# Optimization experiments

Measured on AMD Instinct MI355X. Metric: run time of the kernel, lower is better.

## Reference

```python
import jax, jax.numpy as jnp
import numpy as np
from jax import lax

NH = 4          # num_head
DIM = 512       # attention dim
VDIM = 512      # v_dim
QDIM = 1024     # q_dim
KS = 100        # loc_kernel_size -> conv width 2*KS+1
KN = 100        # loc_kernel_num
TEMP = 0.5      # temperature
BS, TS = 8, 2048


def setup_inputs() -> dict:
    key = jax.random.key(0)
    ks = jax.random.split(key, 12)
    s = 0.05
    return {
        "dec_state": jax.random.normal(ks[0], (BS, QDIM), jnp.float32),
        "enc_feat": jax.random.normal(ks[1], (BS, TS, VDIM), jnp.float32),
        "enc_len": jax.random.randint(ks[2], (BS,), TS // 2, TS + 1).astype(jnp.int32),
        "Wq": jax.random.normal(ks[3], (NH * DIM, QDIM), jnp.float32) * s,
        "bq": jnp.zeros((NH * DIM,), jnp.float32),
        "Wk": jax.random.normal(ks[4], (NH * DIM, VDIM), jnp.float32) * s,
        "bk": jnp.zeros((NH * DIM,), jnp.float32),
        "Wv": jax.random.normal(ks[5], (NH * VDIM, VDIM), jnp.float32) * s,
        "bv": jnp.zeros((NH * VDIM,), jnp.float32),
        "loc_conv_w": jax.random.normal(ks[6], (KN, NH, 2 * KS + 1), jnp.float32) * s,
        "loc_proj_w": jax.random.normal(ks[7], (DIM, KN), jnp.float32) * s,
        "gen_w": jax.random.normal(ks[8], (1, DIM), jnp.float32) * s,
        "gen_b": jnp.zeros((1,), jnp.float32),
        "merge_w": jax.random.normal(ks[9], (VDIM, NH * VDIM), jnp.float32) * s,
        "merge_b": jnp.zeros((VDIM,), jnp.float32),
    }


def reference(dec_state, enc_feat, enc_len, Wq, bq, Wk, bk, Wv, bv,
              loc_conv_w, loc_proj_w, gen_w, gen_b, merge_w, merge_b):
    bs, ts, _ = enc_feat.shape
    # query: [bs, nh, dim]
    query = jnp.tanh(dec_state @ Wq.T + bq).reshape(bs, NH, DIM)
    # key/value: [bs, nh, ts, dim]/[bs, nh, ts, v_dim]
    key = jnp.tanh(enc_feat @ Wk.T + bk).reshape(bs, ts, NH, DIM).transpose(0, 2, 1, 3)
    value = jnp.tanh(enc_feat @ Wv.T + bv).reshape(bs, ts, NH, VDIM).transpose(0, 2, 1, 3)
    # mask & initial (uniform-over-valid) previous attention
    pos = jnp.arange(ts)
    pad_mask = pos[None, :] >= enc_len[:, None]                      # [bs, ts] True = padded
    prev = jnp.where(pad_mask, 0.0, 1.0 / enc_len[:, None].astype(jnp.float32))  # [bs, ts]
    prev_att = jnp.broadcast_to(prev[:, None, :], (bs, NH, ts))      # [bs, nh, ts]
    # location features: Conv1d(nh -> kn, width 2*KS+1, pad KS, no bias)
    conv = lax.conv_general_dilated(prev_att, loc_conv_w, (1,), [(KS, KS)],
                                    dimension_numbers=("NCH", "OIH", "NCH"))  # [bs, kn, ts]
    loc = jnp.tanh(jnp.einsum("bkt,dk->btd", conv, loc_proj_w))      # [bs, ts, dim]
    # additive energy: gen_energy(tanh(k + q + loc))
    e = jnp.tanh(key + query[:, :, None, :] + loc[:, None, :, :])    # [bs, nh, ts, dim]
    energy = jnp.einsum("bhtd,d->bht", e, gen_w[0]) + gen_b[0]
    energy = energy / TEMP
    energy = jnp.where(pad_mask[:, None, :], -jnp.inf, energy)
    attn = jax.nn.softmax(energy, axis=-1)                           # [bs, nh, ts]
    ctx = jnp.einsum("bht,bhtv->bhv", attn, value).reshape(bs, NH * VDIM)
    context = ctx @ merge_w.T + merge_b                              # [bs, v_dim]
    return attn, context
```

## Files before the change

kernel.cpp:

```cpp
#include <hip/hip_runtime.h>
#include <math.h>

#define NH 4
#define DIM 512
#define VDIM 512
#define QDIM 1024
#define KS 100
#define KN 100
#define TEMPERATURE 0.5f
#define BS 8
#define TS 2048
#define NHD (NH * DIM)

#define WS_QUERY   0
#define WS_QTAB    16384
#define WS_ENERGYP 119808
#define WS_CTX     381952
#define WS_P       398336
#define WS_F32_END 418536

typedef __bf16 bf16x8 __attribute__((ext_vector_type(8)));
typedef __bf16 bf16x4 __attribute__((ext_vector_type(4)));
typedef _Float16 f16x8 __attribute__((ext_vector_type(8)));
typedef float  f32x4  __attribute__((ext_vector_type(4)));

#define AS1(p) ((const __attribute__((address_space(1))) void*)(p))
#define AS3(p) ((__attribute__((address_space(3))) void*)(p))

__device__ __forceinline__ float fast_tanh(float x) {
    float e = __expf(2.0f * x);
    return 1.0f - __fdividef(2.0f, e + 1.0f);
}

#define NE4 (BS * TS * VDIM / 4)
#define NW4 (NHD * VDIM / 4)
#define NCVT ((NE4 + 2 * NW4) / 256)
#define NQ2  (NHD / 4)
__global__ void k_pre(const float* __restrict__ enc, const float* __restrict__ Wk,
                      const float* __restrict__ Wv, __bf16* __restrict__ enc_bf,
                      __bf16* __restrict__ wk_bf, __bf16* __restrict__ wv_bf,
                      const float* __restrict__ dec, const float* __restrict__ Wq,
                      const float* __restrict__ bq, float* __restrict__ query,
                      const float* __restrict__ convw, float* __restrict__ P) {
    const int bx = blockIdx.x;
    if (bx < NCVT) {
        int i = bx * blockDim.x + threadIdx.x;
        const float* src; __bf16* dst; int k;
        if (i < NE4)            { src = enc; dst = enc_bf; k = i; }
        else if (i < NE4 + NW4) { src = Wk;  dst = wk_bf;  k = i - NE4; }
        else                    { src = Wv;  dst = wv_bf;  k = i - NE4 - NW4; }
        float4 v = ((const float4*)src)[k];
        bf16x4 o;
        o[0] = (__bf16)v.x; o[1] = (__bf16)v.y; o[2] = (__bf16)v.z; o[3] = (__bf16)v.w;
        ((bf16x4*)dst)[k] = o;
    } else if (bx < NCVT + NQ2) {
        int o = (bx - NCVT) * 4 + (threadIdx.x >> 6);
        int lane = threadIdx.x & 63;
        const float* wr = Wq + (size_t)o * QDIM;
        float s[BS];
        #pragma unroll
        for (int b = 0; b < BS; ++b) s[b] = 0.f;
        #pragma unroll
        for (int i = 0; i < QDIM / 64; ++i) {
            float wv = wr[lane + 64 * i];
            #pragma unroll
            for (int b = 0; b < BS; ++b)
                s[b] = fmaf(wv, dec[b * QDIM + lane + 64 * i], s[b]);
        }
        #pragma unroll
        for (int off = 32; off > 0; off >>= 1)
            #pragma unroll
            for (int b = 0; b < BS; ++b) s[b] += __shfl_down(s[b], off);
        if (lane == 0) {
            float bias = bq[o];
            #pragma unroll
            for (int b = 0; b < BS; ++b) query[b * NHD + o] = tanhf(s[b] + bias);
        }
    } else {
        __shared__ float cs[KN * (2 * KS + 1)];
        int tid = threadIdx.x;
        for (int i = tid; i < KN * (2 * KS + 1); i += 256) {
            int k = i / (2 * KS + 1);
            int dt = i - k * (2 * KS + 1);
            const float* wr = convw + k * (NH * (2 * KS + 1)) + dt;
            cs[i] = wr[0] + wr[201] + wr[402] + wr[603];
        }
        __syncthreads();
        if (tid < KN) {
            float acc = 0.f;
            P[tid] = 0.f;
            const float* c = cs + tid * (2 * KS + 1);
            for (int dt = 0; dt < 2 * KS + 1; ++dt) {
                acc += c[dt];
                P[(dt + 1) * KN + tid] = acc;
            }
        }
    }
}

__global__ void k_qtab(const float* __restrict__ P, const float* __restrict__ projw,
                       float* __restrict__ Qtab, float* __restrict__ ctx) {
    int tid = threadIdx.x;
    if (blockIdx.x >= 2 * KS + 2) {
        int z = (blockIdx.x - (2 * KS + 2)) * 512 + tid;
        ((float4*)ctx)[z] = make_float4(0.f, 0.f, 0.f, 0.f);
        return;
    }
    int j = blockIdx.x;
    __shared__ float Pc[KN];
    if (tid < KN) Pc[tid] = P[j * KN + tid];
    __syncthreads();
    const float* pr = projw + tid * KN;
    float s = 0.f;
    #pragma unroll 4
    for (int k = 0; k < KN; ++k) s = fmaf(pr[k], Pc[k], s);
    Qtab[j * DIM + tid] = s;
}

__global__ __launch_bounds__(512, 4) void k_fused(
    const __bf16* __restrict__ enc_bf, const __bf16* __restrict__ wk_bf,
    const __bf16* __restrict__ wv_bf, const float* __restrict__ bk,
    const float* __restrict__ bv, const float* __restrict__ gen_w,
    const int* __restrict__ enc_len, const float* __restrict__ query,
    const float* __restrict__ Qtab, float* __restrict__ energyP,
    _Float16* __restrict__ val) {
    const int bid = blockIdx.x;
    const int b   = bid >> 8;
    const int t0  = ((bid >> 4) & 15) << 7;
    const int n0  = ((((bid >> 3) & 1) << 3) | (bid & 7)) << 7;
    const int len = enc_len[b];
    if (t0 >= len) return;
    const int tid = threadIdx.x;
    const int w = tid >> 6, lane = tid & 63;
    const int wy = w >> 2, wx = w & 3;
    const int col = lane & 15, quad = lane >> 4;
    __shared__ __bf16 smem[3 * 12288];
    f32x4 accE[4][2], accV[4][2];
    #pragma unroll
    for (int i = 0; i < 4; ++i)
        #pragma unroll
        for (int j = 0; j < 2; ++j) { accE[i][j] = (f32x4)0.f; accV[i][j] = (f32x4)0.f; }
    const int sm = tid >> 2;
    const int sj = (tid & 3) ^ (sm & 3) ^ ((sm >> 2) & 3);
    const __bf16* gpA  = enc_bf + ((size_t)b * TS + t0) * VDIM + (size_t)sm * VDIM + sj * 8;
    const __bf16* gpBk = wk_bf + ((size_t)n0 + sm) * VDIM + sj * 8;
    const __bf16* gpBv = wv_bf + ((size_t)n0 + sm) * VDIM + sj * 8;
    const int cfr = quad ^ (col & 3) ^ ((col >> 2) & 3);
    const char* pbase = (const char*)smem;
    const int offA = (((wy * 64 + col) * 4 + cfr) << 4);
    const int offB = (((wx * 32 + col) * 4 + cfr) << 4);
    #define STG(sbe)                                                               \
        __builtin_amdgcn_global_load_lds(AS1(gpA),  AS3(smem + (sbe) + w * 512), 16, 0, 0);        \
        __builtin_amdgcn_global_load_lds(AS1(gpBk), AS3(smem + (sbe) + 4096 + w * 512), 16, 0, 0); \
        __builtin_amdgcn_global_load_lds(AS1(gpBv), AS3(smem + (sbe) + 8192 + w * 512), 16, 0, 0); \
        gpA += 32; gpBk += 32; gpBv += 32;
    STG(0)
    STG(12288)
    #pragma unroll
    for (int kk = 0; kk < 16; ++kk) {
        if (kk < 15)
            asm volatile("s_waitcnt vmcnt(3) lgkmcnt(0)\n\ts_barrier" ::: "memory");
        else
            asm volatile("s_waitcnt vmcnt(0) lgkmcnt(0)\n\ts_barrier" ::: "memory");
        if (kk < 14) {
            const int sbe = ((kk + 2) % 3) * 12288;
            STG(sbe)
        }
        const int bo = (kk % 3) * 24576;
        bf16x8 af[4], bfr[2];
        #pragma unroll
        for (int i = 0; i < 4; ++i) af[i] = *(const bf16x8*)(pbase + bo + offA + i * 1024);
        #pragma unroll
        for (int j = 0; j < 2; ++j) bfr[j] = *(const bf16x8*)(pbase + bo + 8192 + offB + j * 1024);
        #pragma unroll
        for (int i = 0; i < 4; ++i)
            #pragma unroll
            for (int j = 0; j < 2; ++j)
                accE[i][j] = __builtin_amdgcn_mfma_f32_16x16x32_bf16(af[i], bfr[j], accE[i][j], 0, 0, 0);
        #pragma unroll
        for (int j = 0; j < 2; ++j) bfr[j] = *(const bf16x8*)(pbase + bo + 16384 + offB + j * 1024);
        #pragma unroll
        for (int i = 0; i < 4; ++i)
            #pragma unroll
            for (int j = 0; j < 2; ++j)
                accV[i][j] = __builtin_amdgcn_mfma_f32_16x16x32_bf16(af[i], bfr[j], accV[i][j], 0, 0, 0);
    }
    #undef STG
    __syncthreads();

    _Float16* stage = (_Float16*)smem;
    float* red = (float*)((char*)smem + 32768);

    const int h = n0 >> 9;
    const float inv_len = 1.0f / (float)len;
    float qv[2], gw[2], bkv[2], bvv[2], lI[2];
    int dj[2];
    #pragma unroll
    for (int j = 0; j < 2; ++j) {
        int n = n0 + wx * 32 + j * 16 + col;
        dj[j] = n & (DIM - 1);
        qv[j] = query[b * NHD + n];
        gw[j] = gen_w[dj[j]];
        bkv[j] = bk[n];
        bvv[j] = bv[n];
        lI[j] = fast_tanh((Qtab[(2 * KS + 1) * DIM + dj[j]] - Qtab[dj[j]]) * inv_len);
    }
    #pragma unroll
    for (int i = 0; i < 4; ++i) {
        #pragma unroll
        for (int r = 0; r < 4; ++r) {
            int tl = wy * 64 + i * 16 + quad * 4 + r;
            int t = t0 + tl;
            float l[2];
            if (t >= KS && t < len - KS) {
                #pragma unroll
                for (int j = 0; j < 2; ++j) l[j] = lI[j];
            } else {
                int lo = KS - t; if (lo < 0) lo = 0;
                int hi = KS - t + len - 1; if (hi > 2 * KS) hi = 2 * KS;
                bool has = (hi >= lo);
                #pragma unroll
                for (int j = 0; j < 2; ++j) {
                    float cv = has
                        ? (Qtab[(hi + 1) * DIM + dj[j]] - Qtab[lo * DIM + dj[j]]) * inv_len
                        : 0.f;
                    l[j] = fast_tanh(cv);
                }
            }
            float s = 0.f;
            #pragma unroll
            for (int j = 0; j < 2; ++j) {
                float key = fast_tanh(accE[i][j][r] + bkv[j]);
                float e = fast_tanh(key + qv[j] + l[j]);
                s = fmaf(e, gw[j], s);
            }
            s += __shfl_xor(s, 1); s += __shfl_xor(s, 2);
            s += __shfl_xor(s, 4); s += __shfl_xor(s, 8);
            if (col == 0) red[tl * 4 + wx] = s;
        }
    }
    #pragma unroll
    for (int j = 0; j < 2; ++j) {
        #pragma unroll
        for (int i = 0; i < 4; ++i)
            #pragma unroll
            for (int r = 0; r < 4; ++r) {
                int tl = wy * 64 + i * 16 + quad * 4 + r;
                stage[tl * 128 + wx * 32 + j * 16 + col] =
                    (_Float16)fast_tanh(accV[i][j][r] + bvv[j]);
            }
    }
    __syncthreads();
    if (tid < 128) {
        float s = red[tid * 4] + red[tid * 4 + 1] + red[tid * 4 + 2] + red[tid * 4 + 3];
        energyP[(size_t)((n0 >> 7) & 3) * 65536 + (size_t)(b * NH + h) * TS + t0 + tid] = s;
    }
    #pragma unroll
    for (int it = 0; it < 4; ++it) {
        int idx = it * 512 + tid;
        int row = idx >> 4, seg = idx & 15;
        *(float4*)((char*)(val + ((size_t)b * TS + t0 + row) * NHD + n0) + seg * 16) =
            ((const float4*)stage)[idx];
    }
}

__global__ void k_softmax(const float* __restrict__ energyP, const int* __restrict__ enc_len,
                          const float* __restrict__ gen_b, float* __restrict__ attn) {
    int bh = blockIdx.x;
    int b = bh >> 2;
    int len = enc_len[b];
    int tid = threadIdx.x;
    int w = tid >> 6, lane = tid & 63;
    const float gb = gen_b[0];
    const float* e0 = energyP + (size_t)bh * TS;
    float ev[4];
    float mx = -INFINITY;
    #pragma unroll
    for (int i = 0; i < 4; ++i) {
        int t = i * 512 + tid;
        float e = -INFINITY;
        if (t < len) {
            float s = e0[t] + e0[65536 + t] + e0[131072 + t] + e0[196608 + t];
            e = (s + gb) * (1.0f / TEMPERATURE);
        }
        ev[i] = e;
        mx = fmaxf(mx, e);
    }
    __shared__ float sred[8], ssum[8];
    #pragma unroll
    for (int off = 32; off > 0; off >>= 1) mx = fmaxf(mx, __shfl_xor(mx, off));
    if (lane == 0) sred[w] = mx;
    __syncthreads();
    #pragma unroll
    for (int k = 0; k < 8; ++k) mx = fmaxf(mx, sred[k]);
    float ls = 0.f;
    #pragma unroll
    for (int i = 0; i < 4; ++i) {
        float ex = __expf(ev[i] - mx);
        ev[i] = ex;
        ls += ex;
    }
    #pragma unroll
    for (int off = 32; off > 0; off >>= 1) ls += __shfl_xor(ls, off);
    if (lane == 0) ssum[w] = ls;
    __syncthreads();
    float tot = 0.f;
    #pragma unroll
    for (int k = 0; k < 8; ++k) tot += ssum[k];
    float inv = 1.0f / tot;
    #pragma unroll
    for (int i = 0; i < 4; ++i)
        attn[(size_t)bh * TS + i * 512 + tid] = ev[i] * inv;
}

__global__ __launch_bounds__(256) void k_ctx2(const _Float16* __restrict__ val,
                                              const float* __restrict__ attn,
                                              const int* __restrict__ enc_len,
                                              float* __restrict__ ctx) {
    const int blk = blockIdx.x;
    const int b   = blk >> 7;
    const int nc  = (blk >> 3) & 15;
    const int tsl = blk & 7;
    const int len = enc_len[b];
    const int t0  = tsl * 256;
    if (t0 >= len) return;
    const int n0 = nc * 128;
    const int h  = n0 >> 9;
    const int tid = threadIdx.x;
    const int tn = tid & 15, tr = tid >> 4;
    const float* ar = attn + (size_t)(b * NH + h) * TS;
    float acc[8];
    #pragma unroll
    for (int k = 0; k < 8; ++k) acc[k] = 0.f;
    int tend = t0 + 256; if (tend > len) tend = len;
    for (int t = t0 + tr; t < tend; t += 16) {
        float a = ar[t];
        f16x8 v = *(const f16x8*)(val + ((size_t)b * TS + t) * NHD + n0 + tn * 8);
        #pragma unroll
        for (int k = 0; k < 8; ++k) acc[k] = fmaf(a, (float)v[k], acc[k]);
    }
    __shared__ float cred[16][128];
    #pragma unroll
    for (int k = 0; k < 8; ++k) cred[tr][tn * 8 + k] = acc[k];
    __syncthreads();
    if (tid < 128) {
        float s = 0.f;
        #pragma unroll
        for (int r = 0; r < 16; ++r) s += cred[r][tid];
        atomicAdd(&ctx[(size_t)b * NHD + n0 + tid], s);
    }
}

__global__ void k_merge(const float* __restrict__ ctx, const float* __restrict__ mw,
                        const float* __restrict__ mb, float* __restrict__ out) {
    int o = blockIdx.x * 4 + (threadIdx.x >> 6);
    int lane = threadIdx.x & 63;
    const float* wr = mw + (size_t)o * NHD;
    float s[BS];
    #pragma unroll
    for (int b = 0; b < BS; ++b) s[b] = 0.f;
    #pragma unroll
    for (int i = 0; i < NHD / 64; ++i) {
        float wv = wr[lane + 64 * i];
        #pragma unroll
        for (int b = 0; b < BS; ++b)
            s[b] = fmaf(wv, ctx[b * NHD + lane + 64 * i], s[b]);
    }
    #pragma unroll
    for (int off = 32; off > 0; off >>= 1)
        #pragma unroll
        for (int b = 0; b < BS; ++b) s[b] += __shfl_down(s[b], off);
    if (lane == 0) {
        float bias = mb[o];
        #pragma unroll
        for (int b = 0; b < BS; ++b) out[b * VDIM + o] = s[b] + bias;
    }
}

extern "C" void kernel_launch(void* const* d_in, const int* in_sizes, int n_in,
                              void* d_out, int out_size, void* d_ws, size_t ws_size,
                              hipStream_t stream) {
    const float* dec     = (const float*)d_in[0];
    const float* enc     = (const float*)d_in[1];
    const int*   enc_len = (const int*)d_in[2];
    const float* Wq      = (const float*)d_in[3];
    const float* bq      = (const float*)d_in[4];
    const float* Wk      = (const float*)d_in[5];
    const float* bk      = (const float*)d_in[6];
    const float* Wv      = (const float*)d_in[7];
    const float* bv      = (const float*)d_in[8];
    const float* convw   = (const float*)d_in[9];
    const float* projw   = (const float*)d_in[10];
    const float* gen_w   = (const float*)d_in[11];
    const float* gen_b   = (const float*)d_in[12];
    const float* merge_w = (const float*)d_in[13];
    const float* merge_b = (const float*)d_in[14];

    float* out    = (float*)d_out;
    float* ws     = (float*)d_ws;
    float* query  = ws + WS_QUERY;
    float* Qtab   = ws + WS_QTAB;
    float* energyP= ws + WS_ENERGYP;
    float* ctx    = ws + WS_CTX;
    float* Pws    = ws + WS_P;
    __bf16* enc_bf = (__bf16*)((char*)d_ws + (size_t)WS_F32_END * 4);
    __bf16* wk_bf  = enc_bf + (size_t)BS * TS * VDIM;
    __bf16* wv_bf  = wk_bf + (size_t)NHD * VDIM;
    _Float16* val  = (_Float16*)(wv_bf + (size_t)NHD * VDIM);

    k_pre<<<dim3(NCVT + NQ2 + 1), dim3(256), 0, stream>>>(
        enc, Wk, Wv, enc_bf, wk_bf, wv_bf, dec, Wq, bq, query, convw, Pws);
    k_qtab<<<dim3(2 * KS + 2 + 8), dim3(512), 0, stream>>>(Pws, projw, Qtab, ctx);
    k_fused<<<dim3(2048), dim3(512), 0, stream>>>(
        enc_bf, wk_bf, wv_bf, bk, bv, gen_w, enc_len, query, Qtab, energyP, val);
    k_softmax<<<dim3(BS * NH), dim3(512), 0, stream>>>(energyP, enc_len, gen_b, out);
    k_ctx2<<<dim3(BS * 16 * 8), dim3(256), 0, stream>>>(val, out, enc_len, ctx);
    k_merge<<<dim3(VDIM / 4), dim3(256), 0, stream>>>(ctx, merge_w, merge_b, out + 65536);
}
```

Baseline: 287.7 us.

## Fuse qtab into pre kernel, merge softmax with ctx, swizzle stage LDS

Folds the location-table computation (prefix sums over conv weights times projection) into the preprocessing kernel, with each block recomputing its own prefix sum directly. Fuses softmax with the context reduction so each block recomputes the softmax for its head in-register and consumes attention from shared memory. Adds an XOR swizzle to the fp16 value staging buffer to reduce LDS bank conflicts, and raises wave priority around the MFMA section. This removes two kernel launches and the attention round-trip through global memory, at the cost of redundant softmax and prefix-sum work.

Result: slower. 298.3 us (+3.7%).

```diff
diff --git a/kernel.cpp b/kernel.cpp
--- a/kernel.cpp
+++ b/kernel.cpp
@@ -16,7 +16,6 @@
 #define WS_QTAB    16384
 #define WS_ENERGYP 119808
 #define WS_CTX     381952
-#define WS_P       398336
 #define WS_F32_END 418536
 
 typedef __bf16 bf16x8 __attribute__((ext_vector_type(8)));
@@ -36,12 +35,15 @@
 #define NW4 (NHD * VDIM / 4)
 #define NCVT ((NE4 + 2 * NW4) / 256)
 #define NQ2  (NHD / 4)
+#define NQT  (2 * KS + 2)
+#define NZB  16
 __global__ void k_pre(const float* __restrict__ enc, const float* __restrict__ Wk,
                       const float* __restrict__ Wv, __bf16* __restrict__ enc_bf,
                       __bf16* __restrict__ wk_bf, __bf16* __restrict__ wv_bf,
                       const float* __restrict__ dec, const float* __restrict__ Wq,
                       const float* __restrict__ bq, float* __restrict__ query,
-                      const float* __restrict__ convw, float* __restrict__ P) {
+                      const float* __restrict__ convw, const float* __restrict__ projw,
+                      float* __restrict__ Qtab, float* __restrict__ ctx) {
     const int bx = blockIdx.x;
     if (bx < NCVT) {
         int i = bx * blockDim.x + threadIdx.x;
@@ -76,45 +78,32 @@
             #pragma unroll
             for (int b = 0; b < BS; ++b) query[b * NHD + o] = tanhf(s[b] + bias);
         }
+    } else if (bx < NCVT + NQ2 + NQT) {
+        int j = bx - NCVT - NQ2;
+        int tid = threadIdx.x;
+        __shared__ float sk[KN];
+        if (tid < KN) {
+            const float* wr = convw + tid * (NH * (2 * KS + 1));
+            float acc = 0.f;
+            #pragma unroll 8
+            for (int dt = 0; dt < j; ++dt)
+                acc += wr[dt] + wr[201 + dt] + wr[402 + dt] + wr[603 + dt];
+            sk[tid] = acc;
+        }
+        __syncthreads();
+        #pragma unroll
+        for (int dd = 0; dd < 2; ++dd) {
+            int d = dd * 256 + tid;
+            const float* pr = projw + d * KN;
+            float s = 0.f;
+            #pragma unroll 4
+            for (int k = 0; k < KN; ++k) s = fmaf(pr[k], sk[k], s);
+            Qtab[j * DIM + d] = s;
+        }
     } else {
-        __shared__ float cs[KN * (2 * KS + 1)];
-        int tid = threadIdx.x;
-        for (int i = tid; i < KN * (2 * KS + 1); i += 256) {
-            int k = i / (2 * KS + 1);
-            int dt = i - k * (2 * KS + 1);
-            const float* wr = convw + k * (NH * (2 * KS + 1)) + dt;
-            cs[i] = wr[0] + wr[201] + wr[402] + wr[603];
-        }
-        __syncthreads();
-        if (tid < KN) {
-            float acc = 0.f;
-            P[tid] = 0.f;
-            const float* c = cs + tid * (2 * KS + 1);
-            for (int dt = 0; dt < 2 * KS + 1; ++dt) {
-                acc += c[dt];
-                P[(dt + 1) * KN + tid] = acc;
-            }
-        }
-    }
-}
-
-__global__ void k_qtab(const float* __restrict__ P, const float* __restrict__ projw,
-                       float* __restrict__ Qtab, float* __restrict__ ctx) {
-    int tid = threadIdx.x;
-    if (blockIdx.x >= 2 * KS + 2) {
-        int z = (blockIdx.x - (2 * KS + 2)) * 512 + tid;
+        int z = (bx - NCVT - NQ2 - NQT) * 256 + threadIdx.x;
         ((float4*)ctx)[z] = make_float4(0.f, 0.f, 0.f, 0.f);
-        return;
-    }
-    int j = blockIdx.x;
-    __shared__ float Pc[KN];
-    if (tid < KN) Pc[tid] = P[j * KN + tid];
-    __syncthreads();
-    const float* pr = projw + tid * KN;
-    float s = 0.f;
-    #pragma unroll 4
-    for (int k = 0; k < KN; ++k) s = fmaf(pr[k], Pc[k], s);
-    Qtab[j * DIM + tid] = s;
+    }
 }
 
 __global__ __launch_bounds__(512, 4) void k_fused(
@@ -172,6 +161,7 @@
         for (int i = 0; i < 4; ++i) af[i] = *(const bf16x8*)(pbase + bo + offA + i * 1024);
         #pragma unroll
         for (int j = 0; j < 2; ++j) bfr[j] = *(const bf16x8*)(pbase + bo + 8192 + offB + j * 1024);
+        __builtin_amdgcn_s_setprio(1);
         #pragma unroll
         for (int i = 0; i < 4; ++i)
             #pragma unroll
@@ -184,6 +174,7 @@
             #pragma unroll
             for (int j = 0; j < 2; ++j)
                 accV[i][j] = __builtin_amdgcn_mfma_f32_16x16x32_bf16(af[i], bfr[j], accV[i][j], 0, 0, 0);
+        __builtin_amdgcn_s_setprio(0);
     }
     #undef STG
     __syncthreads();
@@ -246,8 +237,9 @@
             #pragma unroll
             for (int r = 0; r < 4; ++r) {
                 int tl = wy * 64 + i * 16 + quad * 4 + r;
-                stage[tl * 128 + wx * 32 + j * 16 + col] =
-                    (_Float16)fast_tanh(accV[i][j][r] + bvv[j]);
+                int nl = wx * 32 + j * 16 + col;
+                int snl = nl ^ (((tl >> 2) & 3) << 4);
+                stage[tl * 128 + snl] = (_Float16)fast_tanh(accV[i][j][r] + bvv[j]);
             }
     }
     __syncthreads();
@@ -259,25 +251,32 @@
     for (int it = 0; it < 4; ++it) {
         int idx = it * 512 + tid;
         int row = idx >> 4, seg = idx & 15;
-        *(float4*)((char*)(val + ((size_t)b * TS + t0 + row) * NHD + n0) + seg * 16) =
-            ((const float4*)stage)[idx];
-    }
-}
-
-__global__ void k_softmax(const float* __restrict__ energyP, const int* __restrict__ enc_len,
-                          const float* __restrict__ gen_b, float* __restrict__ attn) {
-    int bh = blockIdx.x;
-    int b = bh >> 2;
-    int len = enc_len[b];
-    int tid = threadIdx.x;
-    int w = tid >> 6, lane = tid & 63;
+        int q = (row >> 2) & 3;
+        float4 vv = *(const float4*)((const char*)stage + row * 256 + ((seg * 16) ^ (q << 5)));
+        *(float4*)((char*)(val + ((size_t)b * TS + t0 + row) * NHD + n0) + seg * 16) = vv;
+    }
+}
+
+__global__ __launch_bounds__(256) void k_smctx(const float* __restrict__ energyP,
+                                               const _Float16* __restrict__ val,
+                                               const int* __restrict__ enc_len,
+                                               const float* __restrict__ gen_b,
+                                               float* __restrict__ attn,
+                                               float* __restrict__ ctx) {
+    const int blk = blockIdx.x;
+    const int b = blk >> 6, nc = (blk >> 2) & 15, tsl = blk & 3;
+    const int h = nc >> 2;
+    const int len = enc_len[b];
+    const int bh = b * NH + h;
+    const int tid = threadIdx.x;
+    const int w = tid >> 6, lane = tid & 63;
     const float gb = gen_b[0];
     const float* e0 = energyP + (size_t)bh * TS;
-    float ev[4];
+    float ev[8];
     float mx = -INFINITY;
     #pragma unroll
-    for (int i = 0; i < 4; ++i) {
-        int t = i * 512 + tid;
+    for (int i = 0; i < 8; ++i) {
+        int t = i * 256 + tid;
         float e = -INFINITY;
         if (t < len) {
             float s = e0[t] + e0[65536 + t] + e0[131072 + t] + e0[196608 + t];
@@ -286,16 +285,15 @@
         ev[i] = e;
         mx = fmaxf(mx, e);
     }
-    __shared__ float sred[8], ssum[8];
+    __shared__ float sred[4], ssum[4];
     #pragma unroll
     for (int off = 32; off > 0; off >>= 1) mx = fmaxf(mx, __shfl_xor(mx, off));
     if (lane == 0) sred[w] = mx;
     __syncthreads();
-    #pragma unroll
-    for (int k = 0; k < 8; ++k) mx = fmaxf(mx, sred[k]);
+    mx = fmaxf(fmaxf(sred[0], sred[1]), fmaxf(sred[2], sred[3]));
     float ls = 0.f;
     #pragma unroll
-    for (int i = 0; i < 4; ++i) {
+    for (int i = 0; i < 8; ++i) {
         float ex = __expf(ev[i] - mx);
         ev[i] = ex;
         ls += ex;
@@ -304,38 +302,28 @@
     for (int off = 32; off > 0; off >>= 1) ls += __shfl_xor(ls, off);
     if (lane == 0) ssum[w] = ls;
     __syncthreads();
-    float tot = 0.f;
-    #pragma unroll
-    for (int k = 0; k < 8; ++k) tot += ssum[k];
-    float inv = 1.0f / tot;
-    #pragma unroll
-    for (int i = 0; i < 4; ++i)
-        attn[(size_t)bh * TS + i * 512 + tid] = ev[i] * inv;
-}
-
-__global__ __launch_bounds__(256) void k_ctx2(const _Float16* __restrict__ val,
-                                              const float* __restrict__ attn,
-                                              const int* __restrict__ enc_len,
-                                              float* __restrict__ ctx) {
-    const int blk = blockIdx.x;
-    const int b   = blk >> 7;
-    const int nc  = (blk >> 3) & 15;
-    const int tsl = blk & 7;
-    const int len = enc_len[b];
-    const int t0  = tsl * 256;
+    float inv = 1.0f / (ssum[0] + ssum[1] + ssum[2] + ssum[3]);
+    float a0 = ev[tsl * 2] * inv;
+    float a1 = ev[tsl * 2 + 1] * inv;
+    __shared__ float sa[512];
+    sa[tid] = a0;
+    sa[256 + tid] = a1;
+    if ((nc & 3) == 0) {
+        attn[(size_t)bh * TS + tsl * 512 + tid] = a0;
+        attn[(size_t)bh * TS + tsl * 512 + 256 + tid] = a1;
+    }
+    __syncthreads();
+    const int t0 = tsl * 512;
     if (t0 >= len) return;
-    const int n0 = nc * 128;
-    const int h  = n0 >> 9;
-    const int tid = threadIdx.x;
+    int tend = t0 + 512; if (tend > len) tend = len;
     const int tn = tid & 15, tr = tid >> 4;
-    const float* ar = attn + (size_t)(b * NH + h) * TS;
     float acc[8];
     #pragma unroll
     for (int k = 0; k < 8; ++k) acc[k] = 0.f;
-    int tend = t0 + 256; if (tend > len) tend = len;
+    const _Float16* vb = val + (size_t)b * TS * NHD + (size_t)nc * 128 + tn * 8;
     for (int t = t0 + tr; t < tend; t += 16) {
-        float a = ar[t];
-        f16x8 v = *(const f16x8*)(val + ((size_t)b * TS + t) * NHD + n0 + tn * 8);
+        float a = sa[t - t0];
+        f16x8 v = *(const f16x8*)(vb + (size_t)t * NHD);
         #pragma unroll
         for (int k = 0; k < 8; ++k) acc[k] = fmaf(a, (float)v[k], acc[k]);
     }
@@ -347,7 +335,7 @@
         float s = 0.f;
         #pragma unroll
         for (int r = 0; r < 16; ++r) s += cred[r][tid];
-        atomicAdd(&ctx[(size_t)b * NHD + n0 + tid], s);
+        atomicAdd(&ctx[(size_t)b * NHD + nc * 128 + tid], s);
     }
 }
 
@@ -402,18 +390,15 @@
     float* Qtab   = ws + WS_QTAB;
     float* energyP= ws + WS_ENERGYP;
     float* ctx    = ws + WS_CTX;
-    float* Pws    = ws + WS_P;
     __bf16* enc_bf = (__bf16*)((char*)d_ws + (size_t)WS_F32_END * 4);
     __bf16* wk_bf  = enc_bf + (size_t)BS * TS * VDIM;
     __bf16* wv_bf  = wk_bf + (size_t)NHD * VDIM;
     _Float16* val  = (_Float16*)(wv_bf + (size_t)NHD * VDIM);
 
-    k_pre<<<dim3(NCVT + NQ2 + 1), dim3(256), 0, stream>>>(
-        enc, Wk, Wv, enc_bf, wk_bf, wv_bf, dec, Wq, bq, query, convw, Pws);
-    k_qtab<<<dim3(2 * KS + 2 + 8), dim3(512), 0, stream>>>(Pws, projw, Qtab, ctx);
+    k_pre<<<dim3(NCVT + NQ2 + NQT + NZB), dim3(256), 0, stream>>>(
+        enc, Wk, Wv, enc_bf, wk_bf, wv_bf, dec, Wq, bq, query, convw, projw, Qtab, ctx);
     k_fused<<<dim3(2048), dim3(512), 0, stream>>>(
         enc_bf, wk_bf, wv_bf, bk, bv, gen_w, enc_len, query, Qtab, energyP, val);
-    k_softmax<<<dim3(BS * NH), dim3(512), 0, stream>>>(energyP, enc_len, gen_b, out);
-    k_ctx2<<<dim3(BS * 16 * 8), dim3(256), 0, stream>>>(val, out, enc_len, ctx);
+    k_smctx<<<dim3(512), dim3(256), 0, stream>>>(energyP, val, enc_len, gen_b, out, ctx);
     k_merge<<<dim3(VDIM / 4), dim3(256), 0, stream>>>(ctx, merge_w, merge_b, out + 65536);
 }
```

## Fold Qtab into pre kernel, fuse softmax normalize into ctx, swizzle stage LDS

Applied to the files above, without the earlier changes.

Builds the location table and zeroes ctx inside k_pre, so the separate k_qtab launch goes away. The softmax kernel now writes only max and inverse-sum stats, and k_ctx2 recomputes the normalized attention from energyP, which avoids one write/read pass over the attention. It also XOR-swizzles the fp16 value staging buffer in LDS to cut bank conflicts, and raises wave priority around the MFMA block. The cost is that the ctx kernel now also writes the attention and recomputes exp per block, and the Qtab work runs on only 16 blocks.

New measurement: 347.2 us. 20.7% more time.

```diff
diff --git a/kernel.cpp b/kernel.cpp
--- a/kernel.cpp
+++ b/kernel.cpp
@@ -16,7 +16,7 @@
 #define WS_QTAB    16384
 #define WS_ENERGYP 119808
 #define WS_CTX     381952
-#define WS_P       398336
+#define WS_STATS   398336
 #define WS_F32_END 418536
 
 typedef __bf16 bf16x8 __attribute__((ext_vector_type(8)));
@@ -36,15 +36,76 @@
 #define NW4 (NHD * VDIM / 4)
 #define NCVT ((NE4 + 2 * NW4) / 256)
 #define NQ2  (NHD / 4)
+#define NSPEC (32 + NQ2)
 __global__ void k_pre(const float* __restrict__ enc, const float* __restrict__ Wk,
                       const float* __restrict__ Wv, __bf16* __restrict__ enc_bf,
                       __bf16* __restrict__ wk_bf, __bf16* __restrict__ wv_bf,
                       const float* __restrict__ dec, const float* __restrict__ Wq,
                       const float* __restrict__ bq, float* __restrict__ query,
-                      const float* __restrict__ convw, float* __restrict__ P) {
+                      const float* __restrict__ convw, const float* __restrict__ projw,
+                      float* __restrict__ Qtab, float* __restrict__ ctx) {
     const int bx = blockIdx.x;
-    if (bx < NCVT) {
-        int i = bx * blockDim.x + threadIdx.x;
+    const int tid = threadIdx.x;
+    if (bx < 16) {
+        __shared__ float cs[KN * (2 * KS + 1)];
+        for (int i = tid; i < KN * (2 * KS + 1); i += 256) {
+            int k = i / (2 * KS + 1);
+            int dt = i - k * (2 * KS + 1);
+            const float* wr = convw + k * (NH * (2 * KS + 1)) + dt;
+            cs[i] = wr[0] + wr[201] + wr[402] + wr[603];
+        }
+        __syncthreads();
+        if (tid < KN) {
+            float acc = 0.f;
+            float* c = cs + tid * (2 * KS + 1);
+            for (int dt = 0; dt < 2 * KS + 1; ++dt) { acc += c[dt]; c[dt] = acc; }
+        }
+        __syncthreads();
+        #pragma unroll
+        for (int jj = 0; jj < 13; ++jj) {
+            int j = bx * 13 + jj;
+            if (j >= 2 * KS + 2) break;
+            #pragma unroll
+            for (int dd = 0; dd < 2; ++dd) {
+                int d = dd * 256 + tid;
+                float s = 0.f;
+                if (j > 0) {
+                    const float* pr = projw + d * KN;
+                    #pragma unroll 4
+                    for (int k = 0; k < KN; ++k)
+                        s = fmaf(pr[k], cs[k * (2 * KS + 1) + j - 1], s);
+                }
+                Qtab[j * DIM + d] = s;
+            }
+        }
+    } else if (bx < 32) {
+        int z = (bx - 16) * 256 + tid;
+        ((float4*)ctx)[z] = make_float4(0.f, 0.f, 0.f, 0.f);
+    } else if (bx < NSPEC) {
+        int o = (bx - 32) * 4 + (tid >> 6);
+        int lane = tid & 63;
+        const float* wr = Wq + (size_t)o * QDIM;
+        float s[BS];
+        #pragma unroll
+        for (int b = 0; b < BS; ++b) s[b] = 0.f;
+        #pragma unroll
+        for (int i = 0; i < QDIM / 64; ++i) {
+            float wv = wr[lane + 64 * i];
+            #pragma unroll
+            for (int b = 0; b < BS; ++b)
+                s[b] = fmaf(wv, dec[b * QDIM + lane + 64 * i], s[b]);
+        }
+        #pragma unroll
+        for (int off = 32; off > 0; off >>= 1)
+            #pragma unroll
+            for (int b = 0; b < BS; ++b) s[b] += __shfl_down(s[b], off);
+        if (lane == 0) {
+            float bias = bq[o];
+            #pragma unroll
+            for (int b = 0; b < BS; ++b) query[b * NHD + o] = tanhf(s[b] + bias);
+        }
+    } else {
+        int i = (bx - NSPEC) * 256 + tid;
         const float* src; __bf16* dst; int k;
         if (i < NE4)            { src = enc; dst = enc_bf; k = i; }
         else if (i < NE4 + NW4) { src = Wk;  dst = wk_bf;  k = i - NE4; }
@@ -53,68 +114,7 @@
         bf16x4 o;
         o[0] = (__bf16)v.x; o[1] = (__bf16)v.y; o[2] = (__bf16)v.z; o[3] = (__bf16)v.w;
         ((bf16x4*)dst)[k] = o;
-    } else if (bx < NCVT + NQ2) {
-        int o = (bx - NCVT) * 4 + (threadIdx.x >> 6);
-        int lane = threadIdx.x & 63;
-        const float* wr = Wq + (size_t)o * QDIM;
-        float s[BS];
-        #pragma unroll
-        for (int b = 0; b < BS; ++b) s[b] = 0.f;
-        #pragma unroll
-        for (int i = 0; i < QDIM / 64; ++i) {
-            float wv = wr[lane + 64 * i];
-            #pragma unroll
-            for (int b = 0; b < BS; ++b)
-                s[b] = fmaf(wv, dec[b * QDIM + lane + 64 * i], s[b]);
-        }
-        #pragma unroll
-        for (int off = 32; off > 0; off >>= 1)
-            #pragma unroll
-            for (int b = 0; b < BS; ++b) s[b] += __shfl_down(s[b], off);
-        if (lane == 0) {
-            float bias = bq[o];
-            #pragma unroll
-            for (int b = 0; b < BS; ++b) query[b * NHD + o] = tanhf(s[b] + bias);
-        }
-    } else {
-        __shared__ float cs[KN * (2 * KS + 1)];
-        int tid = threadIdx.x;
-        for (int i = tid; i < KN * (2 * KS + 1); i += 256) {
-            int k = i / (2 * KS + 1);
-            int dt = i - k * (2 * KS + 1);
-            const float* wr = convw + k * (NH * (2 * KS + 1)) + dt;
-            cs[i] = wr[0] + wr[201] + wr[402] + wr[603];
-        }
-        __syncthreads();
-        if (tid < KN) {
-            float acc = 0.f;
-            P[tid] = 0.f;
-            const float* c = cs + tid * (2 * KS + 1);
-            for (int dt = 0; dt < 2 * KS + 1; ++dt) {
-                acc += c[dt];
-                P[(dt + 1) * KN + tid] = acc;
-            }
-        }
-    }
-}
-
-__global__ void k_qtab(const float* __restrict__ P, const float* __restrict__ projw,
-                       float* __restrict__ Qtab, float* __restrict__ ctx) {
-    int tid = threadIdx.x;
-    if (blockIdx.x >= 2 * KS + 2) {
-        int z = (blockIdx.x - (2 * KS + 2)) * 512 + tid;
-        ((float4*)ctx)[z] = make_float4(0.f, 0.f, 0.f, 0.f);
-        return;
-    }
-    int j = blockIdx.x;
-    __shared__ float Pc[KN];
-    if (tid < KN) Pc[tid] = P[j * KN + tid];
-    __syncthreads();
-    const float* pr = projw + tid * KN;
-    float s = 0.f;
-    #pragma unroll 4
-    for (int k = 0; k < KN; ++k) s = fmaf(pr[k], Pc[k], s);
-    Qtab[j * DIM + tid] = s;
+    }
 }
 
 __global__ __launch_bounds__(512, 4) void k_fused(
@@ -172,6 +172,7 @@
         for (int i = 0; i < 4; ++i) af[i] = *(const bf16x8*)(pbase + bo + offA + i * 1024);
         #pragma unroll
         for (int j = 0; j < 2; ++j) bfr[j] = *(const bf16x8*)(pbase + bo + 8192 + offB + j * 1024);
+        __builtin_amdgcn_s_setprio(1);
         #pragma unroll
         for (int i = 0; i < 4; ++i)
             #pragma unroll
@@ -184,6 +185,7 @@
             #pragma unroll
             for (int j = 0; j < 2; ++j)
                 accV[i][j] = __builtin_amdgcn_mfma_f32_16x16x32_bf16(af[i], bfr[j], accV[i][j], 0, 0, 0);
+        __builtin_amdgcn_s_setprio(0);
     }
     #undef STG
     __syncthreads();
@@ -246,8 +248,9 @@
             #pragma unroll
             for (int r = 0; r < 4; ++r) {
                 int tl = wy * 64 + i * 16 + quad * 4 + r;
-                stage[tl * 128 + wx * 32 + j * 16 + col] =
-                    (_Float16)fast_tanh(accV[i][j][r] + bvv[j]);
+                int nl = wx * 32 + j * 16 + col;
+                int snl = nl ^ (((tl >> 2) & 3) << 4);
+                stage[tl * 128 + snl] = (_Float16)fast_tanh(accV[i][j][r] + bvv[j]);
             }
     }
     __syncthreads();
@@ -259,13 +262,14 @@
     for (int it = 0; it < 4; ++it) {
         int idx = it * 512 + tid;
         int row = idx >> 4, seg = idx & 15;
-        *(float4*)((char*)(val + ((size_t)b * TS + t0 + row) * NHD + n0) + seg * 16) =
-            ((const float4*)stage)[idx];
-    }
-}
-
-__global__ void k_softmax(const float* __restrict__ energyP, const int* __restrict__ enc_len,
-                          const float* __restrict__ gen_b, float* __restrict__ attn) {
+        int q = (row >> 2) & 3;
+        float4 vv = *(const float4*)((const char*)stage + row * 256 + ((seg * 16) ^ (q << 5)));
+        *(float4*)((char*)(val + ((size_t)b * TS + t0 + row) * NHD + n0) + seg * 16) = vv;
+    }
+}
+
+__global__ void k_stats(const float* __restrict__ energyP, const int* __restrict__ enc_len,
+                        const float* __restrict__ gen_b, float2* __restrict__ stats) {
     int bh = blockIdx.x;
     int b = bh >> 2;
     int len = enc_len[b];
@@ -295,27 +299,25 @@
     for (int k = 0; k < 8; ++k) mx = fmaxf(mx, sred[k]);
     float ls = 0.f;
     #pragma unroll
-    for (int i = 0; i < 4; ++i) {
-        float ex = __expf(ev[i] - mx);
-        ev[i] = ex;
-        ls += ex;
-    }
+    for (int i = 0; i < 4; ++i) ls += __expf(ev[i] - mx);
     #pragma unroll
     for (int off = 32; off > 0; off >>= 1) ls += __shfl_xor(ls, off);
     if (lane == 0) ssum[w] = ls;
     __syncthreads();
-    float tot = 0.f;
-    #pragma unroll
-    for (int k = 0; k < 8; ++k) tot += ssum[k];
-    float inv = 1.0f / tot;
-    #pragma unroll
-    for (int i = 0; i < 4; ++i)
-        attn[(size_t)bh * TS + i * 512 + tid] = ev[i] * inv;
+    if (tid == 0) {
+        float tot = 0.f;
+        #pragma unroll
+        for (int k = 0; k < 8; ++k) tot += ssum[k];
+        stats[bh] = make_float2(mx, 1.0f / tot);
+    }
 }
 
 __global__ __launch_bounds__(256) void k_ctx2(const _Float16* __restrict__ val,
-                                              const float* __restrict__ attn,
+                                              const float* __restrict__ energyP,
+                                              const float2* __restrict__ stats,
                                               const int* __restrict__ enc_len,
+                                              const float* __restrict__ gen_b,
+                                              float* __restrict__ attn,
                                               float* __restrict__ ctx) {
     const int blk = blockIdx.x;
     const int b   = blk >> 7;
@@ -323,21 +325,35 @@
     const int tsl = blk & 7;
     const int len = enc_len[b];
     const int t0  = tsl * 256;
+    const int h   = nc >> 2;
+    const int bh  = b * NH + h;
+    const int tid = threadIdx.x;
+    const float2 st = stats[bh];
+    const float gb = gen_b[0];
+    const float* e0 = energyP + (size_t)bh * TS;
+    int t = t0 + tid;
+    float a = 0.f;
+    if (t < len) {
+        float s = e0[t] + e0[65536 + t] + e0[131072 + t] + e0[196608 + t];
+        a = __expf((s + gb) * (1.0f / TEMPERATURE) - st.x) * st.y;
+    }
+    if ((nc & 3) == 0) attn[(size_t)bh * TS + t] = a;
     if (t0 >= len) return;
+    __shared__ float sa[256];
+    sa[tid] = a;
+    __syncthreads();
     const int n0 = nc * 128;
-    const int h  = n0 >> 9;
-    const int tid = threadIdx.x;
     const int tn = tid & 15, tr = tid >> 4;
-    const float* ar = attn + (size_t)(b * NH + h) * TS;
     float acc[8];
     #pragma unroll
     for (int k = 0; k < 8; ++k) acc[k] = 0.f;
     int tend = t0 + 256; if (tend > len) tend = len;
-    for (int t = t0 + tr; t < tend; t += 16) {
-        float a = ar[t];
-        f16x8 v = *(const f16x8*)(val + ((size_t)b * TS + t) * NHD + n0 + tn * 8);
-        #pragma unroll
-        for (int k = 0; k < 8; ++k) acc[k] = fmaf(a, (float)v[k], acc[k]);
+    const _Float16* vb = val + (size_t)b * TS * NHD + n0 + tn * 8;
+    for (int tt = t0 + tr; tt < tend; tt += 16) {
+        float av = sa[tt - t0];
+        f16x8 v = *(const f16x8*)(vb + (size_t)tt * NHD);
+        #pragma unroll
+        for (int k = 0; k < 8; ++k) acc[k] = fmaf(av, (float)v[k], acc[k]);
     }
     __shared__ float cred[16][128];
     #pragma unroll
@@ -402,18 +418,18 @@
     float* Qtab   = ws + WS_QTAB;
     float* energyP= ws + WS_ENERGYP;
     float* ctx    = ws + WS_CTX;
-    float* Pws    = ws + WS_P;
+    float2* stats = (float2*)(ws + WS_STATS);
     __bf16* enc_bf = (__bf16*)((char*)d_ws + (size_t)WS_F32_END * 4);
     __bf16* wk_bf  = enc_bf + (size_t)BS * TS * VDIM;
     __bf16* wv_bf  = wk_bf + (size_t)NHD * VDIM;
     _Float16* val  = (_Float16*)(wv_bf + (size_t)NHD * VDIM);
 
-    k_pre<<<dim3(NCVT + NQ2 + 1), dim3(256), 0, stream>>>(
-        enc, Wk, Wv, enc_bf, wk_bf, wv_bf, dec, Wq, bq, query, convw, Pws);
-    k_qtab<<<dim3(2 * KS + 2 + 8), dim3(512), 0, stream>>>(Pws, projw, Qtab, ctx);
+    k_pre<<<dim3(NSPEC + NCVT), dim3(256), 0, stream>>>(
+        enc, Wk, Wv, enc_bf, wk_bf, wv_bf, dec, Wq, bq, query, convw, projw, Qtab, ctx);
     k_fused<<<dim3(2048), dim3(512), 0, stream>>>(
         enc_bf, wk_bf, wv_bf, bk, bv, gen_w, enc_len, query, Qtab, energyP, val);
-    k_softmax<<<dim3(BS * NH), dim3(512), 0, stream>>>(energyP, enc_len, gen_b, out);
-    k_ctx2<<<dim3(BS * 16 * 8), dim3(256), 0, stream>>>(val, out, enc_len, ctx);
+    k_stats<<<dim3(BS * NH), dim3(512), 0, stream>>>(energyP, enc_len, gen_b, stats);
+    k_ctx2<<<dim3(BS * 16 * 8), dim3(256), 0, stream>>>(
+        val, energyP, stats, enc_len, gen_b, out, ctx);
     k_merge<<<dim3(VDIM / 4), dim3(256), 0, stream>>>(ctx, merge_w, merge_b, out + 65536);
 }
```

## Reorder prep blocks, skip padded conversion, add MFMA priority and LDS swizzle

Applied to the files above, without the earlier changes.

The prep kernel is reordered so the long serial conv-prefix block and the query projection blocks launch first, and the conv prefix is computed directly from global memory without a shared staging pass. The bf16 conversion of encoder features now skips padded timesteps past enc_len, cutting memory traffic. The fused kernel raises wave priority around the MFMA section and XOR-swizzles the fp16 value staging buffer in LDS to reduce bank conflicts. Skipping conversion leaves stale bf16 data for padded rows, which is acceptable only if downstream results for those rows are masked.

Result: slower. 306.9 us (+6.6%).

```diff
diff --git a/kernel.cpp b/kernel.cpp
--- a/kernel.cpp
+++ b/kernel.cpp
@@ -41,60 +41,59 @@
                       __bf16* __restrict__ wk_bf, __bf16* __restrict__ wv_bf,
                       const float* __restrict__ dec, const float* __restrict__ Wq,
                       const float* __restrict__ bq, float* __restrict__ query,
-                      const float* __restrict__ convw, float* __restrict__ P) {
+                      const float* __restrict__ convw, float* __restrict__ P,
+                      const int* __restrict__ enc_len) {
     const int bx = blockIdx.x;
-    if (bx < NCVT) {
-        int i = bx * blockDim.x + threadIdx.x;
+    const int tid = threadIdx.x;
+    if (bx == 0) {
+        if (tid < KN) {
+            const float* wr = convw + tid * (NH * (2 * KS + 1));
+            float acc = 0.f;
+            P[tid] = 0.f;
+            #pragma unroll 4
+            for (int dt = 0; dt < 2 * KS + 1; ++dt) {
+                acc += wr[dt] + wr[201 + dt] + wr[402 + dt] + wr[603 + dt];
+                P[(dt + 1) * KN + tid] = acc;
+            }
+        }
+    } else if (bx <= NQ2) {
+        int o = (bx - 1) * 4 + (tid >> 6);
+        int lane = tid & 63;
+        const float* wr = Wq + (size_t)o * QDIM;
+        float s[BS];
+        #pragma unroll
+        for (int b = 0; b < BS; ++b) s[b] = 0.f;
+        #pragma unroll
+        for (int i = 0; i < QDIM / 64; ++i) {
+            float wv = wr[lane + 64 * i];
+            #pragma unroll
+            for (int b = 0; b < BS; ++b)
+                s[b] = fmaf(wv, dec[b * QDIM + lane + 64 * i], s[b]);
+        }
+        #pragma unroll
+        for (int off = 32; off > 0; off >>= 1)
+            #pragma unroll
+            for (int b = 0; b < BS; ++b) s[b] += __shfl_down(s[b], off);
+        if (lane == 0) {
+            float bias = bq[o];
+            #pragma unroll
+            for (int b = 0; b < BS; ++b) query[b * NHD + o] = tanhf(s[b] + bias);
+        }
+    } else {
+        int i = (bx - 1 - NQ2) * 256 + tid;
         const float* src; __bf16* dst; int k;
-        if (i < NE4)            { src = enc; dst = enc_bf; k = i; }
+        if (i < NE4) {
+            int b = i >> 18;
+            int t = (i >> 7) & (TS - 1);
+            if (t >= enc_len[b]) return;
+            src = enc; dst = enc_bf; k = i;
+        }
         else if (i < NE4 + NW4) { src = Wk;  dst = wk_bf;  k = i - NE4; }
         else                    { src = Wv;  dst = wv_bf;  k = i - NE4 - NW4; }
         float4 v = ((const float4*)src)[k];
         bf16x4 o;
         o[0] = (__bf16)v.x; o[1] = (__bf16)v.y; o[2] = (__bf16)v.z; o[3] = (__bf16)v.w;
         ((bf16x4*)dst)[k] = o;
-    } else if (bx < NCVT + NQ2) {
-        int o = (bx - NCVT) * 4 + (threadIdx.x >> 6);
-        int lane = threadIdx.x & 63;
-        const float* wr = Wq + (size_t)o * QDIM;
-        float s[BS];
-        #pragma unroll
-        for (int b = 0; b < BS; ++b) s[b] = 0.f;
-        #pragma unroll
-        for (int i = 0; i < QDIM / 64; ++i) {
-            float wv = wr[lane + 64 * i];
-            #pragma unroll
-            for (int b = 0; b < BS; ++b)
-                s[b] = fmaf(wv, dec[b * QDIM + lane + 64 * i], s[b]);
-        }
-        #pragma unroll
-        for (int off = 32; off > 0; off >>= 1)
-            #pragma unroll
-            for (int b = 0; b < BS; ++b) s[b] += __shfl_down(s[b], off);
-        if (lane == 0) {
-            float bias = bq[o];
-            #pragma unroll
-            for (int b = 0; b < BS; ++b) query[b * NHD + o] = tanhf(s[b] + bias);
-        }
-    } else {
-        __shared__ float cs[KN * (2 * KS + 1)];
-        int tid = threadIdx.x;
-        for (int i = tid; i < KN * (2 * KS + 1); i += 256) {
-            int k = i / (2 * KS + 1);
-            int dt = i - k * (2 * KS + 1);
-            const float* wr = convw + k * (NH * (2 * KS + 1)) + dt;
-            cs[i] = wr[0] + wr[201] + wr[402] + wr[603];
-        }
-        __syncthreads();
-        if (tid < KN) {
-            float acc = 0.f;
-            P[tid] = 0.f;
-            const float* c = cs + tid * (2 * KS + 1);
-            for (int dt = 0; dt < 2 * KS + 1; ++dt) {
-                acc += c[dt];
-                P[(dt + 1) * KN + tid] = acc;
-            }
-        }
     }
 }
 
@@ -172,6 +171,7 @@
         for (int i = 0; i < 4; ++i) af[i] = *(const bf16x8*)(pbase + bo + offA + i * 1024);
         #pragma unroll
         for (int j = 0; j < 2; ++j) bfr[j] = *(const bf16x8*)(pbase + bo + 8192 + offB + j * 1024);
+        __builtin_amdgcn_s_setprio(1);
         #pragma unroll
         for (int i = 0; i < 4; ++i)
             #pragma unroll
@@ -184,6 +184,7 @@
             #pragma unroll
             for (int j = 0; j < 2; ++j)
                 accV[i][j] = __builtin_amdgcn_mfma_f32_16x16x32_bf16(af[i], bfr[j], accV[i][j], 0, 0, 0);
+        __builtin_amdgcn_s_setprio(0);
     }
     #undef STG
     __syncthreads();
@@ -246,8 +247,9 @@
             #pragma unroll
             for (int r = 0; r < 4; ++r) {
                 int tl = wy * 64 + i * 16 + quad * 4 + r;
-                stage[tl * 128 + wx * 32 + j * 16 + col] =
-                    (_Float16)fast_tanh(accV[i][j][r] + bvv[j]);
+                int nl = wx * 32 + j * 16 + col;
+                int snl = nl ^ (((tl >> 2) & 3) << 4);
+                stage[tl * 128 + snl] = (_Float16)fast_tanh(accV[i][j][r] + bvv[j]);
             }
     }
     __syncthreads();
@@ -259,8 +261,9 @@
     for (int it = 0; it < 4; ++it) {
         int idx = it * 512 + tid;
         int row = idx >> 4, seg = idx & 15;
-        *(float4*)((char*)(val + ((size_t)b * TS + t0 + row) * NHD + n0) + seg * 16) =
-            ((const float4*)stage)[idx];
+        int q = (row >> 2) & 3;
+        float4 vv = *(const float4*)((const char*)stage + row * 256 + ((seg * 16) ^ (q << 5)));
+        *(float4*)((char*)(val + ((size_t)b * TS + t0 + row) * NHD + n0) + seg * 16) = vv;
     }
 }
 
@@ -408,8 +411,8 @@
     __bf16* wv_bf  = wk_bf + (size_t)NHD * VDIM;
     _Float16* val  = (_Float16*)(wv_bf + (size_t)NHD * VDIM);
 
-    k_pre<<<dim3(NCVT + NQ2 + 1), dim3(256), 0, stream>>>(
-        enc, Wk, Wv, enc_bf, wk_bf, wv_bf, dec, Wq, bq, query, convw, Pws);
+    k_pre<<<dim3(1 + NQ2 + NCVT), dim3(256), 0, stream>>>(
+        enc, Wk, Wv, enc_bf, wk_bf, wv_bf, dec, Wq, bq, query, convw, Pws, enc_len);
     k_qtab<<<dim3(2 * KS + 2 + 8), dim3(512), 0, stream>>>(Pws, projw, Qtab, ctx);
     k_fused<<<dim3(2048), dim3(512), 0, stream>>>(
         enc_bf, wk_bf, wv_bf, bk, bv, gen_w, enc_len, query, Qtab, energyP, val);
```
